# Optimization experiments

Hardware: AMD Instinct MI355X
Metric: run time of the kernel (lower is better)

## Reference

```python
import jax, jax.numpy as jnp
import numpy as np

NEG = -1e9

def setup_inputs() -> dict:
    key = jax.random.key(0)
    ks = jax.random.split(key, 8)
    B, Lc, Lq, D = 64, 1024, 128, 128
    C = jax.random.normal(ks[0], (B, Lc, D), dtype=jnp.float32)
    Q = jax.random.normal(ks[1], (B, Lq, D), dtype=jnp.float32)
    Cmask = jax.random.randint(ks[2], (B, Lc), 0, 2, dtype=jnp.int32)
    Qmask = jax.random.randint(ks[3], (B, Lq), 0, 2, dtype=jnp.int32)
    w_c = jax.random.normal(ks[4], (D, 1), dtype=jnp.float32) * (6.0 / (D + 1)) ** 0.5
    w_q = jax.random.normal(ks[5], (D, 1), dtype=jnp.float32) * (6.0 / (D + 1)) ** 0.5
    w_mul = jax.random.normal(ks[6], (1, 1, D), dtype=jnp.float32) * (6.0 / (D + 1)) ** 0.5
    bias = jnp.zeros((1,), dtype=jnp.float32)
    return {"C": C, "Q": Q, "Cmask": Cmask, "Qmask": Qmask,
            "w_c": w_c, "w_q": w_q, "w_mul": w_mul, "bias": bias}

def reference(C, Q, Cmask, Qmask, w_c, w_q, w_mul, bias):
    # Optimized trilinear similarity: S[b,i,j] = C.w_c + Q.w_q + (C*w_mul).Q^T + bias
    s0 = jnp.matmul(C, w_c)                        # [B,Lc,1]
    s1 = jnp.swapaxes(jnp.matmul(Q, w_q), 1, 2)    # [B,1,Lq]
    s2 = jnp.einsum('bid,bjd->bij', C * w_mul, Q)  # [B,Lc,Lq]
    S = s0 + s1 + s2 + bias
    qmask = (Qmask[:, None, :] == 0)               # [B,1,Lq]
    cmask = (Cmask[:, :, None] == 0)               # [B,Lc,1]
    S1 = jax.nn.softmax(jnp.where(qmask, NEG, S), axis=2)
    S2 = jax.nn.softmax(jnp.where(cmask, NEG, S), axis=1)
    A = jnp.matmul(S1, Q)                                       # [B,Lc,D]
    Bm = jnp.matmul(jnp.matmul(S1, jnp.swapaxes(S2, 1, 2)), C)  # [B,Lc,D]
    return jnp.concatenate([C, A, C * A, C * Bm], axis=2)
```

## Files before the change

### kernel.cpp

```cpp
#include <hip/hip_runtime.h>
#include <math.h>

constexpr int Bn = 64, Lc = 1024, Lq = 128, Dd = 128;

typedef __attribute__((ext_vector_type(8))) short short8_t;
typedef __attribute__((ext_vector_type(4))) short short4_t;
typedef __attribute__((ext_vector_type(4))) float f32x4;

__device__ __forceinline__ short f2bf(float x) {
    unsigned u = __float_as_uint(x);
    u += 0x7FFFu + ((u >> 16) & 1u);
    return (short)(u >> 16);
}

constexpr int AS = 132;
constexpr int CTS = 68;
constexpr int PS = 68;
constexpr int TBS = 36;

__device__ __forceinline__ void decode_bid(int n, int& b, int& blk) {
    b = (n & 7) * 8 + ((n >> 3) & 7);
    blk = n >> 6;
}

__global__ __launch_bounds__(512) void kT(
    const float* __restrict__ C, const float* __restrict__ Q,
    const int* __restrict__ Cmask, const int* __restrict__ Qmask,
    const float* __restrict__ w_c, const float* __restrict__ w_q,
    const float* __restrict__ w_mul, const float* __restrict__ bias,
    short* __restrict__ Q16, short* __restrict__ QT16,
    float* __restrict__ s1f, short* __restrict__ TT16)
{
    __shared__ short Qs[32 * AS];
    __shared__ short CWs[64 * AS];
    __shared__ short CTs[128 * CTS];
    __shared__ short Ps[32 * PS];
    __shared__ float s1bL[32], qmL[32], invqL[32], s0L[64], cmL[64];
    __shared__ float colAcc[4 * 32];

    int n = blockIdx.x;
    int b, jq; decode_bid(n, b, jq);
    int tid = threadIdx.x, w = tid >> 6, lane = tid & 63;
    int lm = lane & 15, quad = lane >> 4;
    int jh = w & 1, ih = w >> 1;

    {
        int j = tid >> 4, d4 = tid & 15;
        const float4* Q4 = (const float4*)(Q + ((size_t)(b * Lq + jq * 32 + j)) * Dd);
        float4 v0 = Q4[d4], v1 = Q4[d4 + 16];
        short4_t q0, q1;
        q0[0]=f2bf(v0.x); q0[1]=f2bf(v0.y); q0[2]=f2bf(v0.z); q0[3]=f2bf(v0.w);
        q1[0]=f2bf(v1.x); q1[1]=f2bf(v1.y); q1[2]=f2bf(v1.z); q1[3]=f2bf(v1.w);
        *(short4_t*)&Qs[j * AS + d4 * 4] = q0;
        *(short4_t*)&Qs[j * AS + (d4 + 16) * 4] = q1;
        *(short4_t*)&Q16[((size_t)(b * Lq + jq * 32 + j)) * Dd + d4 * 4] = q0;
        *(short4_t*)&Q16[((size_t)(b * Lq + jq * 32 + j)) * Dd + (d4 + 16) * 4] = q1;
        float4 wq0 = ((const float4*)w_q)[d4], wq1 = ((const float4*)w_q)[d4 + 16];
        float dot = v0.x*wq0.x + v0.y*wq0.y + v0.z*wq0.z + v0.w*wq0.w
                  + v1.x*wq1.x + v1.y*wq1.y + v1.z*wq1.z + v1.w*wq1.w;
        #pragma unroll
        for (int off = 1; off < 16; off <<= 1) dot += __shfl_xor(dot, off, 64);
        if (d4 == 0) {
            s1bL[j] = dot + bias[0];
            s1f[b * Lq + jq * 32 + j] = dot;
            qmL[j] = (Qmask[b * Lq + jq * 32 + j] != 0) ? 1.0f : 0.0f;
        }
    }

    const float4* Cb4 = (const float4*)(C + (size_t)b * Lc * Dd);
    int iS = tid >> 5, dS = tid & 31;
    float4 wmv = ((const float4*)w_mul)[dS];
    float4 wcv = ((const float4*)w_c)[dS];
    float4 pc[4]; int pm[4];
    #pragma unroll
    for (int k = 0; k < 4; ++k) {
        pc[k] = Cb4[((size_t)(iS + k * 16)) * 32 + dS];
        pm[k] = Cmask[b * Lc + iS + k * 16];
    }

    float csum[4] = {0.f, 0.f, 0.f, 0.f};
    f32x4 acc2[2];
    acc2[0] = (f32x4){0.f,0.f,0.f,0.f};
    acc2[1] = (f32x4){0.f,0.f,0.f,0.f};

    for (int ic = 0; ic < 16; ++ic) {
        __syncthreads();
        #pragma unroll
        for (int k = 0; k < 4; ++k) {
            float4 v = pc[k];
            float cm = pm[k] ? 1.0f : 0.0f;
            int i = iS + k * 16;
            short4_t cw;
            cw[0]=f2bf(v.x*wmv.x); cw[1]=f2bf(v.y*wmv.y); cw[2]=f2bf(v.z*wmv.z); cw[3]=f2bf(v.w*wmv.w);
            *(short4_t*)&CWs[i * AS + dS * 4] = cw;
            CTs[(dS*4+0)*CTS + i] = f2bf(cm * v.x);
            CTs[(dS*4+1)*CTS + i] = f2bf(cm * v.y);
            CTs[(dS*4+2)*CTS + i] = f2bf(cm * v.z);
            CTs[(dS*4+3)*CTS + i] = f2bf(cm * v.w);
            float dot = v.x*wcv.x + v.y*wcv.y + v.z*wcv.z + v.w*wcv.w;
            #pragma unroll
            for (int off = 1; off < 32; off <<= 1) dot += __shfl_xor(dot, off, 64);
            if (dS == 0) { s0L[i] = dot; cmL[i] = cm; }
        }
        if (ic < 15) {
            int ibn = (ic + 1) * 64;
            #pragma unroll
            for (int k = 0; k < 4; ++k) {
                pc[k] = Cb4[((size_t)(ibn + iS + k * 16)) * 32 + dS];
                pm[k] = Cmask[b * Lc + ibn + iS + k * 16];
            }
        }
        __syncthreads();

        f32x4 sacc = (f32x4){0.f,0.f,0.f,0.f};
        #pragma unroll
        for (int ks = 0; ks < 4; ++ks) {
            short8_t a = *(short8_t*)&Qs[(jh * 16 + lm) * AS + ks * 32 + quad * 8];
            short8_t bq = *(short8_t*)&CWs[(ih * 16 + lm) * AS + ks * 32 + quad * 8];
            sacc = __builtin_amdgcn_mfma_f32_16x16x32_bf16(a, bq, sacc, 0, 0, 0);
        }
        float s0v = s0L[ih * 16 + lm];
        float cmv = cmL[ih * 16 + lm];
        #pragma unroll
        for (int r = 0; r < 4; ++r) {
            float e = __expf(sacc[r] + s0v + s1bL[jh * 16 + quad * 4 + r]);
            Ps[(jh * 16 + quad * 4 + r) * PS + ih * 16 + lm] = f2bf(e);
            csum[r] += cmv * e;
        }
        __syncthreads();

        #pragma unroll
        for (int ks = 0; ks < 2; ++ks) {
            short8_t a = *(short8_t*)&Ps[(jh * 16 + lm) * PS + ks * 32 + quad * 8];
            #pragma unroll
            for (int t = 0; t < 2; ++t) {
                short8_t bf = *(short8_t*)&CTs[((ih * 2 + t) * 16 + lm) * CTS + ks * 32 + quad * 8];
                acc2[t] = __builtin_amdgcn_mfma_f32_16x16x32_bf16(a, bf, acc2[t], 0, 0, 0);
            }
        }
    }

    #pragma unroll
    for (int r = 0; r < 4; ++r) {
        float v = csum[r];
        v += __shfl_xor(v, 1, 64); v += __shfl_xor(v, 2, 64);
        v += __shfl_xor(v, 4, 64); v += __shfl_xor(v, 8, 64);
        if (lm == 0) colAcc[ih * 32 + jh * 16 + quad * 4 + r] = v;
    }
    __syncthreads();
    if (tid < 32) {
        float cs = colAcc[tid] + colAcc[32 + tid] + colAcc[64 + tid] + colAcc[96 + tid];
        invqL[tid] = (qmL[tid] != 0.f) ? 1.0f / cs : 0.0f;
    }
    __syncthreads();

    short* Tb = CWs;
    #pragma unroll
    for (int t = 0; t < 2; ++t) {
        int d = (ih * 2 + t) * 16 + lm;
        #pragma unroll
        for (int r = 0; r < 4; ++r) {
            int jl = jh * 16 + quad * 4 + r;
            Tb[d * TBS + jl] = f2bf(acc2[t][r] * invqL[jl]);
        }
    }
    __syncthreads();
    #pragma unroll
    for (int k = 0; k < 2; ++k) {
        int idx = tid + k * 512;
        int d = idx >> 3, j4 = idx & 7;
        *(short4_t*)&TT16[((size_t)(b * Dd + d)) * Lq + jq * 32 + j4 * 4] =
            *(short4_t*)&Tb[d * TBS + j4 * 4];
    }

    {
        int d = tid >> 2, j8 = (tid & 3) * 8;
        short8_t o;
        #pragma unroll
        for (int r = 0; r < 8; ++r) {
            int j = j8 + r;
            o[r] = (qmL[j] != 0.f) ? Qs[j * AS + d] : (short)0;
        }
        *(short8_t*)&QT16[((size_t)(b * Dd + d)) * Lq + jq * 32 + j8] = o;
    }
}

__global__ __launch_bounds__(256, 3) void k3_out(
    const short* __restrict__ Q16, const short* __restrict__ QT16,
    const short* __restrict__ TT16, const float* __restrict__ C,
    const float* __restrict__ w_mul, const float* __restrict__ w_c,
    const int* __restrict__ Qmask,
    const float* __restrict__ s1f, const float* __restrict__ bias,
    float* __restrict__ out)
{
    __shared__ short Abuf[64 * AS];
    __shared__ short Bbuf[128 * AS];
    __shared__ float s0L[64], s1bL[128], qmLf[128];
    float* Af32 = (float*)Bbuf;

    int n = blockIdx.x;
    int b, blk; decode_bid(n, b, blk);
    int i0 = blk * 64, tid = threadIdx.x;
    int w = tid >> 6, lane = tid & 63, lm = lane & 15, quad = lane >> 4;

    const short8_t* Qg = (const short8_t*)(Q16 + (size_t)b * Lq * Dd);
    #pragma unroll
    for (int k = 0; k < 8; ++k) {
        int idx = tid + k * 256;
        int j = idx >> 4, h = idx & 15;
        *(short8_t*)&Bbuf[j * AS + h * 8] = Qg[idx];
    }
    const float4* C4 = (const float4*)(C + ((size_t)(b * Lc + i0)) * Dd);
    #pragma unroll
    for (int k = 0; k < 8; ++k) {
        int idx = tid + k * 256;
        int i = idx >> 5, d4 = idx & 31;
        float4 v = C4[idx];
        float4 wm = ((const float4*)w_mul)[d4];
        short4_t cw; cw[0]=f2bf(v.x*wm.x); cw[1]=f2bf(v.y*wm.y); cw[2]=f2bf(v.z*wm.z); cw[3]=f2bf(v.w*wm.w);
        *(short4_t*)&Abuf[i * AS + d4 * 4] = cw;
        float4 wc = ((const float4*)w_c)[d4];
        float dot = v.x*wc.x + v.y*wc.y + v.z*wc.z + v.w*wc.w;
        #pragma unroll
        for (int off = 1; off < 32; off <<= 1) dot += __shfl_xor(dot, off, 64);
        if ((tid & 31) == 0) s0L[i] = dot;
    }
    if (tid < 128) {
        s1bL[tid] = s1f[b * Lq + tid] + bias[0];
        qmLf[tid] = (Qmask[b * Lq + tid] != 0) ? 1.0f : 0.0f;
    }
    __syncthreads();

    f32x4 acc[8];
    #pragma unroll
    for (int t = 0; t < 8; ++t) acc[t] = (f32x4){0.f,0.f,0.f,0.f};
    #pragma unroll
    for (int ks = 0; ks < 4; ++ks) {
        short8_t a = *(short8_t*)&Abuf[(w * 16 + lm) * AS + ks * 32 + quad * 8];
        #pragma unroll
        for (int jt = 0; jt < 8; ++jt) {
            short8_t bf = *(short8_t*)&Bbuf[(jt * 16 + lm) * AS + ks * 32 + quad * 8];
            acc[jt] = __builtin_amdgcn_mfma_f32_16x16x32_bf16(a, bf, acc[jt], 0, 0, 0);
        }
    }

    float s0v[4];
    #pragma unroll
    for (int r = 0; r < 4; ++r) s0v[r] = s0L[w * 16 + quad * 4 + r];
    float rowpart[4] = {0.f, 0.f, 0.f, 0.f};
    #pragma unroll
    for (int jt = 0; jt < 8; ++jt) {
        int j = jt * 16 + lm;
        float s1b = s1bL[j];
        float qm = qmLf[j];
        #pragma unroll
        for (int r = 0; r < 4; ++r) {
            float e = __expf(acc[jt][r] + s0v[r] + s1b);
            Abuf[(w * 16 + quad * 4 + r) * AS + j] = f2bf(e);
            rowpart[r] += qm * e;
        }
    }
    float rs[4];
    #pragma unroll
    for (int r = 0; r < 4; ++r) {
        float v = rowpart[r];
        v += __shfl_xor(v, 1, 64); v += __shfl_xor(v, 2, 64);
        v += __shfl_xor(v, 4, 64); v += __shfl_xor(v, 8, 64);
        rs[r] = 1.0f / v;
    }
    __syncthreads();

    const short8_t* QTg = (const short8_t*)(QT16 + (size_t)b * Dd * Lq);
    #pragma unroll
    for (int k = 0; k < 8; ++k) {
        int idx = tid + k * 256;
        int d = idx >> 4, h = idx & 15;
        *(short8_t*)&Bbuf[d * AS + h * 8] = QTg[idx];
    }
    __syncthreads();
    f32x4 accQ[8];
    #pragma unroll
    for (int t = 0; t < 8; ++t) accQ[t] = (f32x4){0.f,0.f,0.f,0.f};
    #pragma unroll
    for (int ks = 0; ks < 4; ++ks) {
        short8_t a = *(short8_t*)&Abuf[(w * 16 + lm) * AS + ks * 32 + quad * 8];
        #pragma unroll
        for (int dt = 0; dt < 8; ++dt) {
            short8_t bf = *(short8_t*)&Bbuf[(dt * 16 + lm) * AS + ks * 32 + quad * 8];
            accQ[dt] = __builtin_amdgcn_mfma_f32_16x16x32_bf16(a, bf, accQ[dt], 0, 0, 0);
        }
    }
    __syncthreads();

    #pragma unroll
    for (int dt = 0; dt < 8; ++dt)
        #pragma unroll
        for (int r = 0; r < 4; ++r)
            Af32[(w * 16 + quad * 4 + r) * AS + dt * 16 + lm] = accQ[dt][r] * rs[r];
    __syncthreads();

    #pragma unroll
    for (int k = 0; k < 8; ++k) {
        int idx = tid + k * 256;
        int i = idx >> 5, d4 = idx & 31;
        float4 av = *(float4*)&Af32[i * AS + d4 * 4];
        float4 c = C4[idx];
        size_t base = ((size_t)(b * Lc + i0 + i)) * (4 * Dd) + d4 * 4;
        *(float4*)&out[base]           = c;
        *(float4*)&out[base + Dd]      = av;
        float4 ca; ca.x = c.x*av.x; ca.y = c.y*av.y; ca.z = c.z*av.z; ca.w = c.w*av.w;
        *(float4*)&out[base + 2 * Dd]  = ca;
    }
    __syncthreads();

    const short8_t* TTg = (const short8_t*)(TT16 + (size_t)b * Dd * Lq);
    #pragma unroll
    for (int k = 0; k < 8; ++k) {
        int idx = tid + k * 256;
        int d = idx >> 4, h = idx & 15;
        *(short8_t*)&Bbuf[d * AS + h * 8] = TTg[idx];
    }
    __syncthreads();
    f32x4 accT[8];
    #pragma unroll
    for (int t = 0; t < 8; ++t) accT[t] = (f32x4){0.f,0.f,0.f,0.f};
    #pragma unroll
    for (int ks = 0; ks < 4; ++ks) {
        short8_t a = *(short8_t*)&Abuf[(w * 16 + lm) * AS + ks * 32 + quad * 8];
        #pragma unroll
        for (int dt = 0; dt < 8; ++dt) {
            short8_t bf = *(short8_t*)&Bbuf[(dt * 16 + lm) * AS + ks * 32 + quad * 8];
            accT[dt] = __builtin_amdgcn_mfma_f32_16x16x32_bf16(a, bf, accT[dt], 0, 0, 0);
        }
    }
    __syncthreads();

    #pragma unroll
    for (int dt = 0; dt < 8; ++dt)
        #pragma unroll
        for (int r = 0; r < 4; ++r)
            Af32[(w * 16 + quad * 4 + r) * AS + dt * 16 + lm] = accT[dt][r] * rs[r];
    __syncthreads();

    #pragma unroll
    for (int k = 0; k < 8; ++k) {
        int idx = tid + k * 256;
        int i = idx >> 5, d4 = idx & 31;
        float4 bm = *(float4*)&Af32[i * AS + d4 * 4];
        float4 c = C4[idx];
        size_t base = ((size_t)(b * Lc + i0 + i)) * (4 * Dd) + d4 * 4;
        float4 cb; cb.x = c.x*bm.x; cb.y = c.y*bm.y; cb.z = c.z*bm.z; cb.w = c.w*bm.w;
        *(float4*)&out[base + 3 * Dd]  = cb;
    }
}

extern "C" void kernel_launch(void* const* d_in, const int* in_sizes, int n_in,
                              void* d_out, int out_size, void* d_ws, size_t ws_size,
                              hipStream_t stream) {
    const float* C     = (const float*)d_in[0];
    const float* Q     = (const float*)d_in[1];
    const int*   Cmask = (const int*)d_in[2];
    const int*   Qmask = (const int*)d_in[3];
    const float* w_c   = (const float*)d_in[4];
    const float* w_q   = (const float*)d_in[5];
    const float* w_mul = (const float*)d_in[6];
    const float* bias  = (const float*)d_in[7];
    float* out = (float*)d_out;

    char* p = (char*)d_ws;
    const size_t NQ = (size_t)Bn * Lq * Dd;
    short* Q16  = (short*)p; p += NQ * 2;
    short* QT16 = (short*)p; p += NQ * 2;
    short* TT16 = (short*)p; p += NQ * 2;
    float* s1f  = (float*)p; p += (size_t)Bn * Lq * 4;

    kT<<<dim3(256), 512, 0, stream>>>(C, Q, Cmask, Qmask, w_c, w_q, w_mul, bias,
                                      Q16, QT16, s1f, TT16);
    k3_out<<<dim3(1024), 256, 0, stream>>>(Q16, QT16, TT16, C, w_mul, w_c, Qmask,
                                           s1f, bias, out);
}
```

Before: 220.3 us.

## Split context reduction in kT across two halves, combine partials in k3_out

The first kernel now launches twice as many blocks, each reducing over half of the context rows. Each block writes fp32 partial T matrices and column sums to workspace. The output kernel sums the two halves, applies the inverse column normalisation, and converts to bf16 when it loads T. This raises occupancy on the serial 16-iteration loop, at the cost of extra fp32 partial traffic (about 8 MB written and heavily re-read). Separately, k3_out keeps C in registers instead of reloading it, which raises register pressure.

```diff
diff --git a/kernel.cpp b/kernel.cpp
--- a/kernel.cpp
+++ b/kernel.cpp
@@ -16,12 +16,7 @@
 constexpr int AS = 132;
 constexpr int CTS = 68;
 constexpr int PS = 68;
-constexpr int TBS = 36;
-
-__device__ __forceinline__ void decode_bid(int n, int& b, int& blk) {
-    b = (n & 7) * 8 + ((n >> 3) & 7);
-    blk = n >> 6;
-}
+constexpr int TBF = 36;
 
 __global__ __launch_bounds__(512) void kT(
     const float* __restrict__ C, const float* __restrict__ Q,
@@ -29,17 +24,18 @@
     const float* __restrict__ w_c, const float* __restrict__ w_q,
     const float* __restrict__ w_mul, const float* __restrict__ bias,
     short* __restrict__ Q16, short* __restrict__ QT16,
-    float* __restrict__ s1f, short* __restrict__ TT16)
+    float* __restrict__ s1f, float* __restrict__ Tpart, float* __restrict__ colpart)
 {
     __shared__ short Qs[32 * AS];
-    __shared__ short CWs[64 * AS];
+    __shared__ short CWs[128 * TBF * 2];
     __shared__ short CTs[128 * CTS];
     __shared__ short Ps[32 * PS];
-    __shared__ float s1bL[32], qmL[32], invqL[32], s0L[64], cmL[64];
-    __shared__ float colAcc[4 * 32];
+    __shared__ float s1bL[32], qmL[32], s0L[64], cmL[64];
+    __shared__ float colAcc[128];
 
     int n = blockIdx.x;
-    int b, jq; decode_bid(n, b, jq);
+    int b = (n & 7) * 8 + ((n >> 3) & 7);
+    int rest = n >> 6, jq = rest & 3, half = rest >> 2;
     int tid = threadIdx.x, w = tid >> 6, lane = tid & 63;
     int lm = lane & 15, quad = lane >> 4;
     int jh = w & 1, ih = w >> 1;
@@ -53,8 +49,10 @@
         q1[0]=f2bf(v1.x); q1[1]=f2bf(v1.y); q1[2]=f2bf(v1.z); q1[3]=f2bf(v1.w);
         *(short4_t*)&Qs[j * AS + d4 * 4] = q0;
         *(short4_t*)&Qs[j * AS + (d4 + 16) * 4] = q1;
-        *(short4_t*)&Q16[((size_t)(b * Lq + jq * 32 + j)) * Dd + d4 * 4] = q0;
-        *(short4_t*)&Q16[((size_t)(b * Lq + jq * 32 + j)) * Dd + (d4 + 16) * 4] = q1;
+        if (half == 0) {
+            *(short4_t*)&Q16[((size_t)(b * Lq + jq * 32 + j)) * Dd + d4 * 4] = q0;
+            *(short4_t*)&Q16[((size_t)(b * Lq + jq * 32 + j)) * Dd + (d4 + 16) * 4] = q1;
+        }
         float4 wq0 = ((const float4*)w_q)[d4], wq1 = ((const float4*)w_q)[d4 + 16];
         float dot = v0.x*wq0.x + v0.y*wq0.y + v0.z*wq0.z + v0.w*wq0.w
                   + v1.x*wq1.x + v1.y*wq1.y + v1.z*wq1.z + v1.w*wq1.w;
@@ -62,8 +60,8 @@
         for (int off = 1; off < 16; off <<= 1) dot += __shfl_xor(dot, off, 64);
         if (d4 == 0) {
             s1bL[j] = dot + bias[0];
-            s1f[b * Lq + jq * 32 + j] = dot;
             qmL[j] = (Qmask[b * Lq + jq * 32 + j] != 0) ? 1.0f : 0.0f;
+            if (half == 0) s1f[b * Lq + jq * 32 + j] = dot;
         }
     }
 
@@ -71,11 +69,13 @@
     int iS = tid >> 5, dS = tid & 31;
     float4 wmv = ((const float4*)w_mul)[dS];
     float4 wcv = ((const float4*)w_c)[dS];
+    int ic0 = half * 8;
     float4 pc[4]; int pm[4];
     #pragma unroll
     for (int k = 0; k < 4; ++k) {
-        pc[k] = Cb4[((size_t)(iS + k * 16)) * 32 + dS];
-        pm[k] = Cmask[b * Lc + iS + k * 16];
+        int gi = ic0 * 64 + iS + k * 16;
+        pc[k] = Cb4[(size_t)gi * 32 + dS];
+        pm[k] = Cmask[b * Lc + gi];
     }
 
     float csum[4] = {0.f, 0.f, 0.f, 0.f};
@@ -83,7 +83,7 @@
     acc2[0] = (f32x4){0.f,0.f,0.f,0.f};
     acc2[1] = (f32x4){0.f,0.f,0.f,0.f};
 
-    for (int ic = 0; ic < 16; ++ic) {
+    for (int ic = ic0; ic < ic0 + 8; ++ic) {
         __syncthreads();
         #pragma unroll
         for (int k = 0; k < 4; ++k) {
@@ -102,7 +102,7 @@
             for (int off = 1; off < 32; off <<= 1) dot += __shfl_xor(dot, off, 64);
             if (dS == 0) { s0L[i] = dot; cmL[i] = cm; }
         }
-        if (ic < 15) {
+        if (ic < ic0 + 7) {
             int ibn = (ic + 1) * 64;
             #pragma unroll
             for (int k = 0; k < 4; ++k) {
@@ -147,33 +147,27 @@
         v += __shfl_xor(v, 4, 64); v += __shfl_xor(v, 8, 64);
         if (lm == 0) colAcc[ih * 32 + jh * 16 + quad * 4 + r] = v;
     }
-    __syncthreads();
-    if (tid < 32) {
-        float cs = colAcc[tid] + colAcc[32 + tid] + colAcc[64 + tid] + colAcc[96 + tid];
-        invqL[tid] = (qmL[tid] != 0.f) ? 1.0f / cs : 0.0f;
-    }
-    __syncthreads();
-
-    short* Tb = CWs;
+    float* Tbf = (float*)CWs;
     #pragma unroll
     for (int t = 0; t < 2; ++t) {
         int d = (ih * 2 + t) * 16 + lm;
         #pragma unroll
-        for (int r = 0; r < 4; ++r) {
-            int jl = jh * 16 + quad * 4 + r;
-            Tb[d * TBS + jl] = f2bf(acc2[t][r] * invqL[jl]);
-        }
-    }
-    __syncthreads();
+        for (int r = 0; r < 4; ++r)
+            Tbf[d * TBF + jh * 16 + quad * 4 + r] = acc2[t][r];
+    }
+    __syncthreads();
+    if (tid < 32)
+        colpart[((size_t)(half * Bn + b)) * Lq + jq * 32 + tid] =
+            colAcc[tid] + colAcc[32 + tid] + colAcc[64 + tid] + colAcc[96 + tid];
     #pragma unroll
     for (int k = 0; k < 2; ++k) {
         int idx = tid + k * 512;
         int d = idx >> 3, j4 = idx & 7;
-        *(short4_t*)&TT16[((size_t)(b * Dd + d)) * Lq + jq * 32 + j4 * 4] =
-            *(short4_t*)&Tb[d * TBS + j4 * 4];
-    }
-
-    {
+        *(float4*)&Tpart[(((size_t)(half * Bn + b)) * Dd + d) * Lq + jq * 32 + j4 * 4] =
+            *(float4*)&Tbf[d * TBF + j4 * 4];
+    }
+
+    if (half == 1) {
         int d = tid >> 2, j8 = (tid & 3) * 8;
         short8_t o;
         #pragma unroll
@@ -187,19 +181,20 @@
 
 __global__ __launch_bounds__(256, 3) void k3_out(
     const short* __restrict__ Q16, const short* __restrict__ QT16,
-    const short* __restrict__ TT16, const float* __restrict__ C,
-    const float* __restrict__ w_mul, const float* __restrict__ w_c,
-    const int* __restrict__ Qmask,
+    const float* __restrict__ Tpart, const float* __restrict__ colpart,
+    const float* __restrict__ C, const float* __restrict__ w_mul,
+    const float* __restrict__ w_c, const int* __restrict__ Qmask,
     const float* __restrict__ s1f, const float* __restrict__ bias,
     float* __restrict__ out)
 {
     __shared__ short Abuf[64 * AS];
     __shared__ short Bbuf[128 * AS];
-    __shared__ float s0L[64], s1bL[128], qmLf[128];
+    __shared__ float s0L[64], s1bL[128], qmLf[128], invqL[128];
     float* Af32 = (float*)Bbuf;
 
     int n = blockIdx.x;
-    int b, blk; decode_bid(n, b, blk);
+    int b = (n & 7) * 8 + ((n >> 3) & 7);
+    int blk = n >> 6;
     int i0 = blk * 64, tid = threadIdx.x;
     int w = tid >> 6, lane = tid & 63, lm = lane & 15, quad = lane >> 4;
 
@@ -211,11 +206,13 @@
         *(short8_t*)&Bbuf[j * AS + h * 8] = Qg[idx];
     }
     const float4* C4 = (const float4*)(C + ((size_t)(b * Lc + i0)) * Dd);
+    float4 cv[8];
     #pragma unroll
     for (int k = 0; k < 8; ++k) {
         int idx = tid + k * 256;
         int i = idx >> 5, d4 = idx & 31;
         float4 v = C4[idx];
+        cv[k] = v;
         float4 wm = ((const float4*)w_mul)[d4];
         short4_t cw; cw[0]=f2bf(v.x*wm.x); cw[1]=f2bf(v.y*wm.y); cw[2]=f2bf(v.z*wm.z); cw[3]=f2bf(v.w*wm.w);
         *(short4_t*)&Abuf[i * AS + d4 * 4] = cw;
@@ -226,8 +223,11 @@
         if ((tid & 31) == 0) s0L[i] = dot;
     }
     if (tid < 128) {
+        float qm = (Qmask[b * Lq + tid] != 0) ? 1.0f : 0.0f;
+        qmLf[tid] = qm;
         s1bL[tid] = s1f[b * Lq + tid] + bias[0];
-        qmLf[tid] = (Qmask[b * Lq + tid] != 0) ? 1.0f : 0.0f;
+        float cs = colpart[(size_t)b * Lq + tid] + colpart[((size_t)(Bn + b)) * Lq + tid];
+        invqL[tid] = (qm != 0.f) ? 1.0f / cs : 0.0f;
     }
     __syncthreads();
 
@@ -304,7 +304,7 @@
         int idx = tid + k * 256;
         int i = idx >> 5, d4 = idx & 31;
         float4 av = *(float4*)&Af32[i * AS + d4 * 4];
-        float4 c = C4[idx];
+        float4 c = cv[k];
         size_t base = ((size_t)(b * Lc + i0 + i)) * (4 * Dd) + d4 * 4;
         *(float4*)&out[base]           = c;
         *(float4*)&out[base + Dd]      = av;
@@ -313,12 +313,19 @@
     }
     __syncthreads();
 
-    const short8_t* TTg = (const short8_t*)(TT16 + (size_t)b * Dd * Lq);
-    #pragma unroll
-    for (int k = 0; k < 8; ++k) {
-        int idx = tid + k * 256;
-        int d = idx >> 4, h = idx & 15;
-        *(short8_t*)&Bbuf[d * AS + h * 8] = TTg[idx];
+    const float4* T0 = (const float4*)(Tpart + (size_t)b * Dd * Lq);
+    const float4* T1 = (const float4*)(Tpart + ((size_t)(Bn + b)) * Dd * Lq);
+    #pragma unroll
+    for (int k = 0; k < 16; ++k) {
+        int idx = tid + k * 256;
+        int d = idx >> 5, j4 = idx & 31;
+        float4 x = T0[idx], y = T1[idx];
+        short4_t o;
+        o[0] = f2bf((x.x + y.x) * invqL[j4 * 4 + 0]);
+        o[1] = f2bf((x.y + y.y) * invqL[j4 * 4 + 1]);
+        o[2] = f2bf((x.z + y.z) * invqL[j4 * 4 + 2]);
+        o[3] = f2bf((x.w + y.w) * invqL[j4 * 4 + 3]);
+        *(short4_t*)&Bbuf[d * AS + j4 * 4] = o;
     }
     __syncthreads();
     f32x4 accT[8];
@@ -347,7 +354,7 @@
         int idx = tid + k * 256;
         int i = idx >> 5, d4 = idx & 31;
         float4 bm = *(float4*)&Af32[i * AS + d4 * 4];
-        float4 c = C4[idx];
+        float4 c = cv[k];
         size_t base = ((size_t)(b * Lc + i0 + i)) * (4 * Dd) + d4 * 4;
         float4 cb; cb.x = c.x*bm.x; cb.y = c.y*bm.y; cb.z = c.z*bm.z; cb.w = c.w*bm.w;
         *(float4*)&out[base + 3 * Dd]  = cb;
@@ -369,13 +376,14 @@
 
     char* p = (char*)d_ws;
     const size_t NQ = (size_t)Bn * Lq * Dd;
-    short* Q16  = (short*)p; p += NQ * 2;
-    short* QT16 = (short*)p; p += NQ * 2;
-    short* TT16 = (short*)p; p += NQ * 2;
-    float* s1f  = (float*)p; p += (size_t)Bn * Lq * 4;
-
-    kT<<<dim3(256), 512, 0, stream>>>(C, Q, Cmask, Qmask, w_c, w_q, w_mul, bias,
-                                      Q16, QT16, s1f, TT16);
-    k3_out<<<dim3(1024), 256, 0, stream>>>(Q16, QT16, TT16, C, w_mul, w_c, Qmask,
+    short* Q16   = (short*)p; p += NQ * 2;
+    short* QT16  = (short*)p; p += NQ * 2;
+    float* Tpart = (float*)p; p += 2 * NQ * 4;
+    float* colpart = (float*)p; p += 2 * (size_t)Bn * Lq * 4;
+    float* s1f   = (float*)p; p += (size_t)Bn * Lq * 4;
+
+    kT<<<dim3(512), 512, 0, stream>>>(C, Q, Cmask, Qmask, w_c, w_q, w_mul, bias,
+                                      Q16, QT16, s1f, Tpart, colpart);
+    k3_out<<<dim3(1024), 256, 0, stream>>>(Q16, QT16, Tpart, colpart, C, w_mul, w_c, Qmask,
                                            s1f, bias, out);
 }
```

Result: faster. 214.6 us (-2.6%).
